# Kernel tuning notes

Hardware: AMD Instinct MI355X
Metric: run time of the kernel (lower is better)

The kernel has to match this reference:

```python
import jax, jax.numpy as jnp
import numpy as np

BITS = 1.58
EPS = 1e-8


def absmean_quantize(w, bits=BITS, scale_method='mean'):
    # gamma over the whole weight tensor (CPU path of original)
    if scale_method == 'mean':
        gamma = jnp.mean(jnp.abs(w))
    else:
        gamma = jnp.max(jnp.abs(w))
    levels = 2.0 ** bits - 1.0  # ~1.989 for 1.58-bit ternary-ish
    half = levels / 2.0
    return jnp.clip(jnp.round(w / (gamma + EPS) * half), -half, half)


def setup_inputs() -> dict:
    key = jax.random.key(0)
    k_x, k_w, k_b = jax.random.split(key, 3)
    B, S, D_IN, D_OUT = 8, 2048, 4096, 4096
    x = jax.random.normal(k_x, (B, S, D_IN), dtype=jnp.float32)
    # kaiming_uniform_(a=sqrt(5)) -> bound = sqrt(6/((1+5)*fan_in)) = 1/sqrt(fan_in)
    bound = 1.0 / np.sqrt(D_IN)
    weight = jax.random.uniform(k_w, (D_OUT, D_IN), minval=-bound, maxval=bound, dtype=jnp.float32)
    bias = jax.random.uniform(k_b, (D_OUT,), minval=-bound, maxval=bound, dtype=jnp.float32)
    return {"x": x, "weight": weight, "bias": bias}


def reference(x, weight, bias):
    qw = absmean_quantize(weight)                      # [D_OUT, D_IN]
    out = jnp.einsum('bsi,oi->bso', x, qw)             # F.linear without bias
    return out + bias
```

## Files before the change

### kernel.cpp

```cpp
#include <hip/hip_runtime.h>
#include <math.h>
#include <stdint.h>


#define MDIM 16384
#define NDIM 4096
#define KDIM 4096

__global__ void absmean_reduce(const float4* __restrict__ w4,
                               double* __restrict__ gsum, int n4) {
  int tid = blockIdx.x * blockDim.x + threadIdx.x;
  int stride = gridDim.x * blockDim.x;
  double s = 0.0;
  for (int i = tid; i < n4; i += stride) {
    float4 v = w4[i];
    s += (double)fabsf(v.x) + (double)fabsf(v.y) +
         (double)fabsf(v.z) + (double)fabsf(v.w);
  }
  for (int off = 32; off > 0; off >>= 1) s += __shfl_down(s, off, 64);
  __shared__ double partial[4];
  int ln = threadIdx.x & 63, wv = threadIdx.x >> 6;
  if (ln == 0) partial[wv] = s;
  __syncthreads();
  if (threadIdx.x == 0) {
    double t = partial[0] + partial[1] + partial[2] + partial[3];
    atomicAdd(gsum, t);
  }
}

__device__ __forceinline__ unsigned short tern_bf16(float w, float g, float h) {
  float q = rintf(w / g * h);
  q = fminf(fmaxf(q, -1.0f), 1.0f);
  return (unsigned short)(__float_as_uint(q) >> 16);
}

__global__ void quantize_w(const float4* __restrict__ w4,
                           const double* __restrict__ gsum,
                           ushort4* __restrict__ wq, int n4, float halfF) {
  const float gamma = (float)(*gsum * (1.0 / 16777216.0)) + 1e-8f;
  int tid = blockIdx.x * blockDim.x + threadIdx.x;
  int stride = gridDim.x * blockDim.x;
  for (int i = tid; i < n4; i += stride) {
    float4 v = w4[i];
    ushort4 o;
    o.x = tern_bf16(v.x, gamma, halfF);
    o.y = tern_bf16(v.y, gamma, halfF);
    o.z = tern_bf16(v.z, gamma, halfF);
    o.w = tern_bf16(v.w, gamma, halfF);
    wq[i] = o;
  }
}

__device__ __forceinline__ unsigned bf16_rne(float f) {
  unsigned u = __float_as_uint(f);
  return (u + 0x7FFFu + ((u >> 16) & 1u)) >> 16;
}
__device__ __forceinline__ unsigned pack2(float lo, float hi) {
  return bf16_rne(lo) | (bf16_rne(hi) << 16);
}

__global__ void cvt_x(const float4* __restrict__ x4, uint4* __restrict__ xb,
                      int n8) {
  int tid = blockIdx.x * blockDim.x + threadIdx.x;
  int stride = gridDim.x * blockDim.x;
  for (int i = tid; i < n8; i += stride) {
    float4 a = x4[2 * i];
    float4 b = x4[2 * i + 1];
    uint4 o;
    o.x = pack2(a.x, a.y);
    o.y = pack2(a.z, a.w);
    o.z = pack2(b.x, b.y);
    o.w = pack2(b.z, b.w);
    xb[i] = o;
  }
}

typedef __attribute__((ext_vector_type(8))) short bf16x8;
typedef __attribute__((ext_vector_type(4))) float f32x4;

#define BM 128
#define BN 128
#define BK 64

__device__ __forceinline__ void async16(const short* g, short* l) {
  __builtin_amdgcn_global_load_lds(
      (const __attribute__((address_space(1))) unsigned int*)g,
      (__attribute__((address_space(3))) unsigned int*)l, 16, 0, 0);
}

__global__ __launch_bounds__(256, 2) void gemm_tern_bf16(
    const short* __restrict__ A,
    const short* __restrict__ Bw,
    const float* __restrict__ bias,
    float* __restrict__ out,
    float scale) {
  __shared__ short As[BM * BK];
  __shared__ short Bs[BN * BK];

  const int tid = threadIdx.x;
  const int wv = tid >> 6;
  const int ln = tid & 63;
  const int bm = blockIdx.y * BM;
  const int bn = blockIdx.x * BN;
  const int wm = (wv >> 1) * 64;
  const int wn = (wv & 1) * 64;

  f32x4 acc[4][4] = {};

  const int srow = ln >> 3;
  const int scol = ((ln & 7) ^ (ln >> 3)) * 8;
  const short* pA = A + (size_t)(bm + wv * 32 + srow) * KDIM + scol;
  const short* pB = Bw + (size_t)(bn + wv * 32 + srow) * KDIM + scol;

  for (int k0 = 0; k0 < KDIM; k0 += BK) {
#pragma unroll
    for (int c = 0; c < 4; ++c) {
      async16(pA + (size_t)(c * 8) * KDIM, As + (wv * 32 + c * 8) * BK);
      async16(pB + (size_t)(c * 8) * KDIM, Bs + (wv * 32 + c * 8) * BK);
    }
    pA += BK;
    pB += BK;
    __syncthreads();

#pragma unroll
    for (int ks = 0; ks < BK; ks += 32) {
      const int ch = ((ks >> 3) + (ln >> 4)) ^ (ln & 7);
      bf16x8 fa[4], fb[4];
#pragma unroll
      for (int t = 0; t < 4; ++t) {
        fa[t] = *(const bf16x8*)(As + (wm + t * 16 + (ln & 15)) * BK + ch * 8);
        fb[t] = *(const bf16x8*)(Bs + (wn + t * 16 + (ln & 15)) * BK + ch * 8);
      }
#pragma unroll
      for (int i = 0; i < 4; ++i)
#pragma unroll
        for (int j = 0; j < 4; ++j)
          acc[i][j] = __builtin_amdgcn_mfma_f32_16x16x32_bf16(
              fa[i], fb[j], acc[i][j], 0, 0, 0);
    }
    __syncthreads();
  }

  const int col0 = bn + wn + (ln & 15);
  const int row0 = bm + wm + ((ln >> 4) << 2);
#pragma unroll
  for (int j = 0; j < 4; ++j) {
    const float bj = bias[col0 + j * 16];
#pragma unroll
    for (int i = 0; i < 4; ++i) {
#pragma unroll
      for (int r = 0; r < 4; ++r) {
        out[(size_t)(row0 + i * 16 + r) * NDIM + (col0 + j * 16)] =
            fmaf(acc[i][j][r], scale, bj);
      }
    }
  }
}

extern "C" void kernel_launch(void* const* d_in, const int* in_sizes, int n_in,
                              void* d_out, int out_size, void* d_ws,
                              size_t ws_size, hipStream_t stream) {
  const float* x = (const float*)d_in[0];
  const float* w = (const float*)d_in[1];
  const float* bias = (const float*)d_in[2];
  float* out = (float*)d_out;

  char* ws = (char*)d_ws;
  double* gsum = (double*)ws;
  short* xb = (short*)(ws + 256);
  short* wq = (short*)(ws + 256 + (size_t)MDIM * KDIM * 2);

  const float kHalfF = (float)((pow(2.0, 1.58) - 1.0) * 0.5);

  hipMemsetAsync(gsum, 0, sizeof(double), stream);

  const int nW4 = (NDIM * KDIM) / 4;
  absmean_reduce<<<1024, 256, 0, stream>>>((const float4*)w, gsum, nW4);

  quantize_w<<<4096, 256, 0, stream>>>((const float4*)w, gsum, (ushort4*)wq,
                                       nW4, kHalfF);

  const int nX8 = (MDIM * KDIM) / 8;
  cvt_x<<<8192, 256, 0, stream>>>((const float4*)x, (uint4*)xb, nX8);

  dim3 grid(NDIM / BN, MDIM / BM);
  gemm_tern_bf16<<<grid, 256, 0, stream>>>(xb, wq, bias, out, kHalfF);
}
```

Before: 972.8 us.

## Rewrite GEMM as 256x256 tile with double-buffered LDS and phased prefetch

Replaces the 128x128 single-buffered GEMM with a 256x256 tile kernel using 512 threads and 128KB of dynamic LDS split into two stages. Each K step runs four quadrant phases that issue async global-to-LDS loads for upcoming stages while MFMAs run, using explicit waitcnt, barriers and setprio. The block index is remapped so neighbouring blocks share tiles in L2. The larger tile raises reuse per byte loaded, at the cost of register and LDS pressure and lower occupancy.

```diff
diff --git a/kernel.cpp b/kernel.cpp
--- a/kernel.cpp
+++ b/kernel.cpp
@@ -78,9 +78,10 @@
 typedef __attribute__((ext_vector_type(8))) short bf16x8;
 typedef __attribute__((ext_vector_type(4))) float f32x4;
 
-#define BM 128
-#define BN 128
+#define BM 256
+#define BN 256
 #define BK 64
+#define NTK (KDIM / BK)
 
 __device__ __forceinline__ void async16(const short* g, short* l) {
   __builtin_amdgcn_global_load_lds(
@@ -88,73 +89,136 @@
       (__attribute__((address_space(3))) unsigned int*)l, 16, 0, 0);
 }
 
-__global__ __launch_bounds__(256, 2) void gemm_tern_bf16(
+__global__ __launch_bounds__(512, 2) void gemm_tern_256(
     const short* __restrict__ A,
     const short* __restrict__ Bw,
     const float* __restrict__ bias,
     float* __restrict__ out,
     float scale) {
-  __shared__ short As[BM * BK];
-  __shared__ short Bs[BN * BK];
+  extern __shared__ short lds[];
 
   const int tid = threadIdx.x;
   const int wv = tid >> 6;
   const int ln = tid & 63;
-  const int bm = blockIdx.y * BM;
-  const int bn = blockIdx.x * BN;
-  const int wm = (wv >> 1) * 64;
-  const int wn = (wv & 1) * 64;
-
-  f32x4 acc[4][4] = {};
-
-  const int srow = ln >> 3;
-  const int scol = ((ln & 7) ^ (ln >> 3)) * 8;
-  const short* pA = A + (size_t)(bm + wv * 32 + srow) * KDIM + scol;
-  const short* pB = Bw + (size_t)(bn + wv * 32 + srow) * KDIM + scol;
-
-  for (int k0 = 0; k0 < KDIM; k0 += BK) {
-#pragma unroll
-    for (int c = 0; c < 4; ++c) {
-      async16(pA + (size_t)(c * 8) * KDIM, As + (wv * 32 + c * 8) * BK);
-      async16(pB + (size_t)(c * 8) * KDIM, Bs + (wv * 32 + c * 8) * BK);
+  const int wr = wv >> 2;
+  const int wc = wv & 3;
+  const int l15 = ln & 15;
+  const int lq = ln >> 4;
+  const int l7 = ln & 7;
+
+  const int orig = blockIdx.x;
+  const int wg = ((orig & 7) << 7) | (orig >> 3);
+  const int bm = (wg >> 4) * BM;
+  const int bn = (wg & 15) * BN;
+
+  const int g8 = ln >> 3;
+  const int sw = (l7 ^ (g8 & 7)) << 3;
+  const int grp0 = wv * 2, grp1 = wv * 2 + 1;
+  const short* aP0 = A + (size_t)(bm + grp0 * 8 + g8) * KDIM + sw;
+  const short* aP1 = A + (size_t)(bm + grp1 * 8 + g8) * KDIM + sw;
+  const short* bP0 = Bw + (size_t)(bn + grp0 * 8 + g8) * KDIM + sw;
+  const short* bP1 = Bw + (size_t)(bn + grp1 * 8 + g8) * KDIM + sw;
+  const int d0 = grp0 * 512, d1 = grp1 * 512;
+
+  int rowA[4], rowB[2], chk[2];
+#pragma unroll
+  for (int m = 0; m < 4; ++m) rowA[m] = (wr * 64 + m * 16 + l15) * 64;
+#pragma unroll
+  for (int n = 0; n < 2; ++n) rowB[n] = (wc * 32 + n * 16 + l15) * 64;
+#pragma unroll
+  for (int ks = 0; ks < 2; ++ks) chk[ks] = (((ks * 4 + lq) ^ l7) << 3);
+
+  f32x4 acc[2][2][4][2] = {};
+
+#define KOF(s) ((size_t)(((s) < NTK) ? (s) : 0) * BK)
+#define STAGE_A(DST, H, S)                              \
+  do {                                                  \
+    const size_t koA_ = KOF(S) + (size_t)(H) * 128 * KDIM; \
+    async16(aP0 + koA_, (DST) + (H) * 8192 + d0);       \
+    async16(aP1 + koA_, (DST) + (H) * 8192 + d1);       \
+  } while (0)
+#define STAGE_B(DST, H, S)                                  \
+  do {                                                      \
+    const size_t koB_ = KOF(S) + (size_t)(H) * 128 * KDIM;  \
+    async16(bP0 + koB_, (DST) + 16384 + (H) * 8192 + d0);   \
+    async16(bP1 + koB_, (DST) + 16384 + (H) * 8192 + d1);   \
+  } while (0)
+
+  {
+    short* b0 = lds;
+    short* b1 = lds + 32768;
+    STAGE_A(b0, 0, 0);
+    STAGE_B(b0, 0, 0);
+    STAGE_B(b0, 1, 0);
+    STAGE_A(b0, 1, 0);
+    STAGE_A(b1, 0, 1);
+    STAGE_B(b1, 0, 1);
+  }
+  asm volatile("s_waitcnt vmcnt(4)" ::: "memory");
+  __builtin_amdgcn_sched_barrier(0);
+  __builtin_amdgcn_s_barrier();
+
+#define PHASE(MH, NH, STAGE_STMT, POST_STMT)                                  \
+  do {                                                                        \
+    bf16x8 fa[4][2], fb[2][2];                                                \
+    const short* Ah_ = C + (MH) * 8192;                                       \
+    const short* Bh_ = C + 16384 + (NH) * 8192;                               \
+    _Pragma("unroll") for (int m = 0; m < 4; ++m) {                           \
+      fa[m][0] = *(const bf16x8*)(Ah_ + rowA[m] + chk[0]);                    \
+      fa[m][1] = *(const bf16x8*)(Ah_ + rowA[m] + chk[1]);                    \
+    }                                                                         \
+    _Pragma("unroll") for (int n = 0; n < 2; ++n) {                           \
+      fb[n][0] = *(const bf16x8*)(Bh_ + rowB[n] + chk[0]);                    \
+      fb[n][1] = *(const bf16x8*)(Bh_ + rowB[n] + chk[1]);                    \
+    }                                                                         \
+    STAGE_STMT;                                                               \
+    __builtin_amdgcn_sched_barrier(0);                                        \
+    __builtin_amdgcn_s_barrier();                                             \
+    asm volatile("s_waitcnt lgkmcnt(0)" ::: "memory");                        \
+    __builtin_amdgcn_sched_barrier(0);                                        \
+    __builtin_amdgcn_s_setprio(1);                                            \
+    _Pragma("unroll") for (int m = 0; m < 4; ++m)                             \
+        _Pragma("unroll") for (int n = 0; n < 2; ++n) {                       \
+      acc[MH][NH][m][n] = __builtin_amdgcn_mfma_f32_16x16x32_bf16(            \
+          fa[m][0], fb[n][0], acc[MH][NH][m][n], 0, 0, 0);                    \
+      acc[MH][NH][m][n] = __builtin_amdgcn_mfma_f32_16x16x32_bf16(            \
+          fa[m][1], fb[n][1], acc[MH][NH][m][n], 0, 0, 0);                    \
+    }                                                                         \
+    __builtin_amdgcn_s_setprio(0);                                            \
+    POST_STMT;                                                                \
+    __builtin_amdgcn_sched_barrier(0);                                        \
+    __builtin_amdgcn_s_barrier();                                             \
+  } while (0)
+
+  for (int kt = 0; kt < NTK; ++kt) {
+    short* C = lds + ((kt & 1) << 15);
+    short* Nx = lds + (((kt & 1) ^ 1) << 15);
+    PHASE(0, 0, STAGE_B(Nx, 1, kt + 1), ((void)0));
+    PHASE(0, 1, STAGE_A(Nx, 1, kt + 1), ((void)0));
+    PHASE(1, 0, STAGE_A(C, 0, kt + 2), ((void)0));
+    PHASE(1, 1, STAGE_B(C, 0, kt + 2),
+          asm volatile("s_waitcnt vmcnt(4)" ::: "memory"));
+  }
+
+  const int colb = bn + wc * 32 + l15;
+  const int rowb = bm + wr * 64 + (lq << 2);
+#pragma unroll
+  for (int nh = 0; nh < 2; ++nh)
+#pragma unroll
+    for (int n = 0; n < 2; ++n) {
+      const int col = colb + nh * 128 + n * 16;
+      const float bj = bias[col];
+#pragma unroll
+      for (int mh = 0; mh < 2; ++mh)
+#pragma unroll
+        for (int m = 0; m < 4; ++m) {
+          const int row = rowb + mh * 128 + m * 16;
+#pragma unroll
+          for (int r = 0; r < 4; ++r)
+            out[(size_t)(row + r) * NDIM + col] =
+                fmaf(acc[mh][nh][m][n][r], scale, bj);
+        }
     }
-    pA += BK;
-    pB += BK;
-    __syncthreads();
-
-#pragma unroll
-    for (int ks = 0; ks < BK; ks += 32) {
-      const int ch = ((ks >> 3) + (ln >> 4)) ^ (ln & 7);
-      bf16x8 fa[4], fb[4];
-#pragma unroll
-      for (int t = 0; t < 4; ++t) {
-        fa[t] = *(const bf16x8*)(As + (wm + t * 16 + (ln & 15)) * BK + ch * 8);
-        fb[t] = *(const bf16x8*)(Bs + (wn + t * 16 + (ln & 15)) * BK + ch * 8);
-      }
-#pragma unroll
-      for (int i = 0; i < 4; ++i)
-#pragma unroll
-        for (int j = 0; j < 4; ++j)
-          acc[i][j] = __builtin_amdgcn_mfma_f32_16x16x32_bf16(
-              fa[i], fb[j], acc[i][j], 0, 0, 0);
-    }
-    __syncthreads();
-  }
-
-  const int col0 = bn + wn + (ln & 15);
-  const int row0 = bm + wm + ((ln >> 4) << 2);
-#pragma unroll
-  for (int j = 0; j < 4; ++j) {
-    const float bj = bias[col0 + j * 16];
-#pragma unroll
-    for (int i = 0; i < 4; ++i) {
-#pragma unroll
-      for (int r = 0; r < 4; ++r) {
-        out[(size_t)(row0 + i * 16 + r) * NDIM + (col0 + j * 16)] =
-            fmaf(acc[i][j][r], scale, bj);
-      }
-    }
-  }
 }
 
 extern "C" void kernel_launch(void* const* d_in, const int* in_sizes, int n_in,
@@ -172,6 +236,14 @@
 
   const float kHalfF = (float)((pow(2.0, 1.58) - 1.0) * 0.5);
 
+  static bool attr_done = false;
+  if (!attr_done) {
+    (void)hipFuncSetAttribute((const void*)gemm_tern_256,
+                              hipFuncAttributeMaxDynamicSharedMemorySize,
+                              131072);
+    attr_done = true;
+  }
+
   hipMemsetAsync(gsum, 0, sizeof(double), stream);
 
   const int nW4 = (NDIM * KDIM) / 4;
@@ -183,6 +255,6 @@
   const int nX8 = (MDIM * KDIM) / 8;
   cvt_x<<<8192, 256, 0, stream>>>((const float4*)x, (uint4*)xb, nX8);
 
-  dim3 grid(NDIM / BN, MDIM / BM);
-  gemm_tern_bf16<<<grid, 256, 0, stream>>>(xb, wq, bias, out, kHalfF);
-}
+  dim3 grid((MDIM / BM) * (NDIM / BN));
+  gemm_tern_256<<<grid, 512, 131072, stream>>>(xb, wq, bias, out, kHalfF);
+}
```

New measurement: 996.6 us. +2.4%, slower.
